# Optimization experiments

Measured on AMD Instinct MI355X. Metric: run time of the kernel, lower is better.

The kernel has to match this reference:

```python
import jax, jax.numpy as jnp
import numpy as np

B, T, D, H, K, V, W = 2, 2048, 768, 12, 64, 64, 1024
EPS = 1e-6


def setup_inputs() -> dict:
    key = jax.random.key(0)
    ks = jax.random.split(key, 10)
    std = 0.02
    return {
        "x": jax.random.normal(ks[0], (B, T, D), jnp.float32),
        "gdn_state": jax.random.normal(ks[1], (B, H, K, V), jnp.float32),
        "Wq": jax.random.normal(ks[2], (D, H * K), jnp.float32) * std,
        "Wk": jax.random.normal(ks[3], (D, H * K), jnp.float32) * std,
        "Wv": jax.random.normal(ks[4], (D, H * K), jnp.float32) * std,
        "Wo": jax.random.normal(ks[5], (H * K, D), jnp.float32) * std,
        "Wgq": jax.random.normal(ks[6], (D, H * K), jnp.float32) * std,
        "Wro": jax.random.normal(ks[7], (H * V, D), jnp.float32) * std,
        "Wg": jax.random.normal(ks[8], (D, H), jnp.float32) * std,
        "bg": jnp.full((H,), 1.0, jnp.float32),  # swa_gate_init
        "norm_w": jnp.ones((D,), jnp.float32),
    }


def reference(x, gdn_state, Wq, Wk, Wv, Wo, Wgq, Wro, Wg, bg, norm_w):
    # RMSNorm
    xn = x * jax.lax.rsqrt(jnp.mean(x * x, axis=-1, keepdims=True) + EPS) * norm_w

    def proj(w):  # (B,T,D)@(D,HK) -> (B,H,T,K)
        return (xn @ w).reshape(B, T, H, K).transpose(0, 2, 1, 3)

    q, k, v = proj(Wq), proj(Wk), proj(Wv)
    scale = K ** -0.5

    scores = jnp.einsum("bhqk,bhsk->bhqs", q, k) * scale  # (B,H,T,T)
    i = jnp.arange(T)[:, None]
    j = jnp.arange(T)[None, :]
    allowed = (j <= i) & (j >= i - W)  # causal sliding window
    scores = jnp.where(allowed, scores, -jnp.inf)
    attn = jax.nn.softmax(scores, axis=-1)

    local = jnp.einsum("bhqs,bhsk->bhqk", attn, v)
    local = local.transpose(0, 2, 1, 3).reshape(B, T, H * K) @ Wo  # (B,T,D)

    # GDN state retrieval
    qg = jax.nn.relu((xn @ Wgq).reshape(B, T, H, K).transpose(0, 2, 1, 3))  # (B,H,T,K)
    retrieved = jnp.einsum("bhkv,bhtk->bhtv", gdn_state, qg)  # (B,H,T,V)
    retrieval = retrieved.transpose(0, 2, 1, 3).reshape(B, T, H * V) @ Wro  # (B,T,D)
    gate = jax.nn.sigmoid(xn @ Wg + bg)  # (B,T,H)
    retrieval = jnp.mean(gate, axis=-1, keepdims=True) * retrieval

    return x + local + retrieval
```

## Files before the change

kernel.cpp:

```cpp
#include <hip/hip_runtime.h>
#include <math.h>
#include <stdint.h>

typedef float f32x4 __attribute__((ext_vector_type(4)));
typedef __bf16 bf16x8 __attribute__((ext_vector_type(8)));
typedef __bf16 bf16x4 __attribute__((ext_vector_type(4)));

constexpr int Bc = 2, Tc = 2048, Dc = 768, Hc = 12, Wc = 1024;
#define CEXP 0.18033688011112042f

__device__ __forceinline__ f32x4 mfma_bf16(bf16x8 a, bf16x8 b, f32x4 c) {
    return __builtin_amdgcn_mfma_f32_16x16x32_bf16(a, b, c, 0, 0, 0);
}
__device__ __forceinline__ void gload16(const void* g, void* l) {
    __builtin_amdgcn_global_load_lds(
        (const __attribute__((address_space(1))) uint32_t*)g,
        (__attribute__((address_space(3))) uint32_t*)l, 16, 0, 0);
}
__device__ __forceinline__ uint32_t pack2(float a, float b) {
    union { __bf16 h[2]; uint32_t u; } x;
    x.h[0] = (__bf16)a; x.h[1] = (__bf16)b; return x.u;
}
__device__ __forceinline__ void s_wait_vm4()   { asm volatile("s_waitcnt vmcnt(4)" ::: "memory"); }
__device__ __forceinline__ void s_wait_vm0()   { asm volatile("s_waitcnt vmcnt(0)" ::: "memory"); }
__device__ __forceinline__ void s_wait_lgkm0() { asm volatile("s_waitcnt lgkmcnt(0)" ::: "memory"); }
__device__ __forceinline__ void bar()          { __builtin_amdgcn_s_barrier(); }

__global__ __launch_bounds__(256) void k_prep_w(
    const float* __restrict__ Wq, const float* __restrict__ Wk,
    const float* __restrict__ Wv, const float* __restrict__ Wgq,
    const float* __restrict__ Wo, const float* __restrict__ Wro,
    __bf16* __restrict__ wTproj, __bf16* __restrict__ wTout)
{
    __shared__ __bf16 ldsT[64][66];
    const int wsel = blockIdx.y;
    const float* srcs[6] = {Wq, Wk, Wv, Wgq, Wo, Wro};
    const float* src = srcs[wsel];
    __bf16* dst; int dstride, koff;
    if (wsel < 4) { dst = wTproj + (size_t)wsel * Dc * Dc; dstride = Dc;  koff = 0; }
    else if (wsel == 4) { dst = wTout; dstride = 1536; koff = 0; }
    else { dst = wTout; dstride = 1536; koff = 768; }
    const float scale = (wsel == 0) ? CEXP : 1.0f;

    int tile = blockIdx.x;
    int tk = tile % 12, tn = tile / 12;
    int k0 = tk * 64, n0 = tn * 64;
    int i = threadIdx.x, rsub = i >> 4, c4 = i & 15;
#pragma unroll
    for (int rep = 0; rep < 4; ++rep) {
        int row = rep * 16 + rsub;
        float4 v = *(const float4*)(src + (size_t)(k0 + row) * Dc + n0 + c4 * 4);
        ldsT[c4 * 4 + 0][row] = (__bf16)(v.x * scale);
        ldsT[c4 * 4 + 1][row] = (__bf16)(v.y * scale);
        ldsT[c4 * 4 + 2][row] = (__bf16)(v.z * scale);
        ldsT[c4 * 4 + 3][row] = (__bf16)(v.w * scale);
    }
    __syncthreads();
#pragma unroll
    for (int rep = 0; rep < 4; ++rep) {
        int n = rep * 16 + rsub;
        bf16x4 o = *(const bf16x4*)&ldsT[n][c4 * 4];
        *(bf16x4*)(dst + (size_t)(n0 + n) * dstride + koff + k0 + c4 * 4) = o;
    }
}

__global__ __launch_bounds__(256) void k_prep_state(
    const float* __restrict__ st, __bf16* __restrict__ stT)
{
    int idx = blockIdx.x * 256 + threadIdx.x;
    int bh = idx >> 12, kk = (idx >> 6) & 63, vv = idx & 63;
    stT[(size_t)bh * 4096 + vv * 64 + kk] = (__bf16)st[idx];
}

__global__ __launch_bounds__(256) void k_rmsnorm(
    const float* __restrict__ x, const float* __restrict__ norm_w,
    __bf16* __restrict__ xnb)
{
    int row = blockIdx.x, tid = threadIdx.x;
    const float* xr = x + (size_t)row * Dc;
    float4 v = make_float4(0.f, 0.f, 0.f, 0.f);
    float ss = 0.f;
    if (tid < 192) {
        v = ((const float4*)xr)[tid];
        ss = v.x * v.x + v.y * v.y + v.z * v.z + v.w * v.w;
    }
#pragma unroll
    for (int m = 32; m; m >>= 1) ss += __shfl_xor(ss, m, 64);
    __shared__ float red[4];
    if ((tid & 63) == 0) red[tid >> 6] = ss;
    __syncthreads();
    float tot = red[0] + red[1] + red[2] + red[3];
    float rms = rsqrtf(tot * (1.f / 768.f) + 1e-6f);
    if (tid < 192) {
        float4 nw = ((const float4*)norm_w)[tid];
        bf16x4 o;
        o[0] = (__bf16)(v.x * rms * nw.x);
        o[1] = (__bf16)(v.y * rms * nw.y);
        o[2] = (__bf16)(v.z * rms * nw.z);
        o[3] = (__bf16)(v.w * rms * nw.w);
        *(bf16x4*)(xnb + (size_t)row * Dc + tid * 4) = o;
    }
}

__global__ __launch_bounds__(256) void k_gate(
    const __bf16* __restrict__ xnb, const float* __restrict__ Wg,
    const float* __restrict__ bg, float* __restrict__ gmean)
{
    int row = blockIdx.x * 4 + (threadIdx.x >> 6);
    int lane = threadIdx.x & 63;
    const __bf16* xr = xnb + (size_t)row * Dc;
    float p[12];
#pragma unroll
    for (int h = 0; h < 12; ++h) p[h] = 0.f;
    for (int d = lane; d < Dc; d += 64) {
        float xv = (float)xr[d];
        const float* wr = Wg + d * 12;
#pragma unroll
        for (int h = 0; h < 12; ++h) p[h] += xv * wr[h];
    }
#pragma unroll
    for (int h = 0; h < 12; ++h) {
#pragma unroll
        for (int m = 32; m; m >>= 1) p[h] += __shfl_xor(p[h], m, 64);
    }
    if (lane == 0) {
        float s = 0.f;
#pragma unroll
        for (int h = 0; h < 12; ++h) s += 1.f / (1.f + expf(-(p[h] + bg[h])));
        gmean[row] = s * (1.f / 12.f);
    }
}

template <int MODE>
__global__ __launch_bounds__(256) void k_gemm(
    const __bf16* __restrict__ A, const __bf16* __restrict__ BT,
    const float* __restrict__ xres, float* __restrict__ outf,
    __bf16* __restrict__ qb, __bf16* __restrict__ kbf,
    __bf16* __restrict__ vtb, __bf16* __restrict__ qgb)
{
    constexpr int BM = (MODE == 0) ? 128 : 64;
    constexpr int BN = (MODE == 0) ? 128 : 64;
    constexpr int KD = (MODE == 0) ? 768 : 1536;
    constexpr int BK = (MODE == 0) ? 32 : 64;
    constexpr int KI = BK / 32;
    constexpr int WM = BM / 2, WN = BN / 2;
    constexpr int MI = WM / 16, NI = WN / 16;
    constexpr int MT = 4096 / BM;
    constexpr int NK = KD / BK;
    constexpr int GR = BK / 8;
    constexpr int ACH = BM * BK / 2048;
    constexpr int BCH = BN * BK / 2048;
    __shared__ __bf16 As[2][BM * BK];
    __shared__ __bf16 Bs[2][BN * BK];
    const int tid = threadIdx.x, w = tid >> 6, lane = tid & 63;
    const int g = lane >> 4, t = lane & 15;
    int id = blockIdx.x, xcd = id & 7, l = id >> 3;
    int nid = xcd * 96 + l;
    int m0 = (nid % MT) * BM, n0 = (nid / MT) * BN;
    const __bf16* Abase = A + (size_t)m0 * KD;
    const __bf16* Bbase = BT + (size_t)n0 * KD;
    const int wrow = (w >> 1) * WM, wcol = (w & 1) * WN;

    auto STAGE = [&](int buf, int k0) {
#pragma unroll
        for (int c = 0; c < ACH; ++c) {
            int chunk = c * 256 + tid, row = chunk / GR, cix = chunk % GR;
            gload16(Abase + (size_t)row * KD + k0 + cix * 8, &As[buf][chunk * 8]);
        }
#pragma unroll
        for (int c = 0; c < BCH; ++c) {
            int chunk = c * 256 + tid, row = chunk / GR, cix = chunk % GR;
            gload16(Bbase + (size_t)row * KD + k0 + cix * 8, &Bs[buf][chunk * 8]);
        }
    };

    f32x4 acc[MI][NI] = {};
    STAGE(0, 0);
    STAGE(1, BK);
    for (int ks = 0; ks < NK; ++ks) {
        if (ks == NK - 1) s_wait_vm0(); else s_wait_vm4();
        bar();
        const __bf16* Ab = As[ks & 1];
        const __bf16* Bb = Bs[ks & 1];
        bf16x8 af[MI][KI], bfr[NI][KI];
#pragma unroll
        for (int kk = 0; kk < KI; ++kk) {
#pragma unroll
            for (int mi = 0; mi < MI; ++mi)
                af[mi][kk] = *(const bf16x8*)(Ab + (wrow + mi * 16 + t) * BK + kk * 32 + g * 8);
#pragma unroll
            for (int ni = 0; ni < NI; ++ni)
                bfr[ni][kk] = *(const bf16x8*)(Bb + (wcol + ni * 16 + t) * BK + kk * 32 + g * 8);
        }
        s_wait_lgkm0();
        __builtin_amdgcn_sched_barrier(0);
        bar();
        if (ks + 2 < NK) STAGE(ks & 1, (ks + 2) * BK);
        __builtin_amdgcn_s_setprio(1);
#pragma unroll
        for (int kk = 0; kk < KI; ++kk)
#pragma unroll
            for (int mi = 0; mi < MI; ++mi)
#pragma unroll
                for (int ni = 0; ni < NI; ++ni)
                    acc[mi][ni] = mfma_bf16(af[mi][kk], bfr[ni][kk], acc[mi][ni]);
        __builtin_amdgcn_s_setprio(0);
    }
    const int region = (MODE == 0) ? (n0 / 768) : 0;
#pragma unroll
    for (int mi = 0; mi < MI; ++mi)
#pragma unroll
        for (int ni = 0; ni < NI; ++ni)
#pragma unroll
            for (int r = 0; r < 4; ++r) {
                int grow = m0 + wrow + mi * 16 + g * 4 + r;
                int gcol = n0 + wcol + ni * 16 + t;
                float v = acc[mi][ni][r];
                if (MODE == 1) {
                    size_t idx = (size_t)grow * Dc + gcol;
                    outf[idx] = xres[idx] + v;
                } else {
                    int c = gcol - region * 768;
                    int h = c >> 6, kd = c & 63;
                    int b = grow >> 11, ti = grow & (Tc - 1);
                    if (region == 0)
                        qb[((size_t)(b * Hc + h) * Tc + ti) * 64 + kd] = (__bf16)v;
                    else if (region == 1) {
                        int kds = kd ^ ((ti & 7) << 3);
                        kbf[((size_t)(b * Hc + h) * Tc + ti) * 64 + kds] = (__bf16)v;
                    } else if (region == 2) {
                        int kap = ti & 63;
                        int rho = (kap & 32) | (((kap >> 2) & 3) << 3) |
                                  (((kap >> 4) & 1) << 2) | (kap & 3);
                        int ts = (ti & ~63) | (rho ^ ((kd & 7) << 3));
                        vtb[((size_t)(b * Hc + h) * 64 + kd) * Tc + ts] = (__bf16)v;
                    } else
                        qgb[((size_t)(b * Hc + h) * Tc + ti) * 64 + kd] = (__bf16)fmaxf(v, 0.f);
                }
            }
}

__global__ __launch_bounds__(256) void k_attn(
    const __bf16* __restrict__ q, const __bf16* __restrict__ k,
    const __bf16* __restrict__ vt, __bf16* __restrict__ ac)
{
    __shared__ __bf16 Ks[2][64 * 64];
    __shared__ __bf16 Vs[2][64 * 64];
    int id = blockIdx.x, xcd = id & 7, l = id >> 3;
    int nid = xcd * 96 + l;
    int sblk = nid & 31, h = (nid >> 5) % Hc, b = nid / (32 * Hc);
    int tid = threadIdx.x;
    int w = tid >> 6, lane = tid & 63;
    int g = lane >> 4, t = lane & 15;
    int q0 = sblk * 64, qw = q0 + w * 16;
    const __bf16* qb = q + (size_t)(b * Hc + h) * Tc * 64;
    const __bf16* kb = k + (size_t)(b * Hc + h) * Tc * 64;
    const __bf16* vb = vt + (size_t)(b * Hc + h) * 64 * Tc;

    bf16x8 qf0 = *(const bf16x8*)(qb + (size_t)(qw + t) * 64 + g * 8);
    bf16x8 qf1 = *(const bf16x8*)(qb + (size_t)(qw + t) * 64 + 32 + g * 8);

    const int qi = qw + t;
    const int lowB = qi - Wc;
    const int xr = t & 7;

    f32x4 oacc[4] = {};
    float lsum = 0.f;

    const int s_begin = (q0 >= Wc) ? q0 - Wc : 0;
    const int s_endq = q0 + 64;

    auto STAGE = [&](int buf, int s0) {
#pragma unroll
        for (int j = 0; j < 2; ++j) {
            int ch = j * 256 + tid;
            gload16(kb + (size_t)(s0 + (ch >> 3)) * 64 + (ch & 7) * 8,
                    &Ks[buf][ch * 8]);
            gload16(vb + (size_t)(ch >> 3) * Tc + s0 + (ch & 7) * 8,
                    &Vs[buf][ch * 8]);
        }
    };

    STAGE(0, s_begin);
    if (s_begin + 64 < s_endq) STAGE(1, s_begin + 64);
    int cur = 0;
    for (int s0 = s_begin; s0 < s_endq; s0 += 64) {
        if (s0 + 64 >= s_endq) s_wait_vm0(); else s_wait_vm4();
        bar();
        const __bf16* Kt = Ks[cur];
        const __bf16* Vt = Vs[cur];
        f32x4 sc[4];
        __builtin_amdgcn_s_setprio(1);
#pragma unroll
        for (int sub = 0; sub < 4; ++sub) {
            const __bf16* kr = Kt + (sub * 16 + t) * 64;
            bf16x8 kA = *(const bf16x8*)(kr + ((g ^ xr) << 3));
            bf16x8 kB = *(const bf16x8*)(kr + (((g + 4) ^ xr) << 3));
            f32x4 s = {};
            s = mfma_bf16(kA, qf0, s);
            s = mfma_bf16(kB, qf1, s);
            sc[sub] = s;
        }
        __builtin_amdgcn_s_setprio(0);
        float pv[4][4];
#pragma unroll
        for (int sub = 0; sub < 4; ++sub)
#pragma unroll
            for (int r = 0; r < 4; ++r) {
                int kk = s0 + sub * 16 + g * 4 + r;
                float e = exp2f(sc[sub][r]);
                float val = (kk <= qi && kk >= lowB) ? e : 0.f;
                pv[sub][r] = val;
                lsum += val;
            }
        __builtin_amdgcn_s_setprio(1);
#pragma unroll
        for (int ks = 0; ks < 2; ++ks) {
            union { uint32_t u[4]; bf16x8 v; } pf;
            pf.u[0] = pack2(pv[ks * 2][0], pv[ks * 2][1]);
            pf.u[1] = pack2(pv[ks * 2][2], pv[ks * 2][3]);
            pf.u[2] = pack2(pv[ks * 2 + 1][0], pv[ks * 2 + 1][1]);
            pf.u[3] = pack2(pv[ks * 2 + 1][2], pv[ks * 2 + 1][3]);
#pragma unroll
            for (int n = 0; n < 4; ++n) {
                const __bf16* vrow = Vt + (n * 16 + t) * 64;
                bf16x8 vf = *(const bf16x8*)(vrow + ((((ks * 4) + g) ^ xr) << 3));
                oacc[n] = mfma_bf16(pf.v, vf, oacc[n]);
            }
        }
        __builtin_amdgcn_s_setprio(0);
        s_wait_lgkm0();
        __builtin_amdgcn_sched_barrier(0);
        bar();
        if (s0 + 128 < s_endq) STAGE(cur, s0 + 128);
        cur ^= 1;
    }
    lsum += __shfl_xor(lsum, 16, 64);
    lsum += __shfl_xor(lsum, 32, 64);
    float linv = 1.f / lsum;
    float lq[4];
#pragma unroll
    for (int r = 0; r < 4; ++r) lq[r] = __shfl(linv, g * 4 + r, 64);
#pragma unroll
    for (int n = 0; n < 4; ++n)
#pragma unroll
        for (int r = 0; r < 4; ++r) {
            int qrow = qw + g * 4 + r;
            ac[(size_t)(b * Tc + qrow) * 1536 + h * 64 + n * 16 + t] =
                (__bf16)(oacc[n][r] * lq[r]);
        }
}

__global__ __launch_bounds__(256) void k_retr(
    const __bf16* __restrict__ qg, const __bf16* __restrict__ stateT,
    const float* __restrict__ gmean, __bf16* __restrict__ ac)
{
    int b = blockIdx.z, h = blockIdx.y;
    int w = threadIdx.x >> 6, lane = threadIdx.x & 63;
    int g = lane >> 4, t = lane & 15;
    int t0 = blockIdx.x * 64 + w * 16;
    const __bf16* qbp = qg + (size_t)(b * Hc + h) * Tc * 64;
    const __bf16* sb = stateT + (size_t)(b * Hc + h) * 64 * 64;
    bf16x8 a0 = *(const bf16x8*)(qbp + (size_t)(t0 + t) * 64 + g * 8);
    bf16x8 a1 = *(const bf16x8*)(qbp + (size_t)(t0 + t) * 64 + 32 + g * 8);
#pragma unroll
    for (int n = 0; n < 4; ++n) {
        bf16x8 b0 = *(const bf16x8*)(sb + (n * 16 + t) * 64 + g * 8);
        bf16x8 b1 = *(const bf16x8*)(sb + (n * 16 + t) * 64 + 32 + g * 8);
        f32x4 acc = {};
        acc = mfma_bf16(a0, b0, acc);
        acc = mfma_bf16(a1, b1, acc);
#pragma unroll
        for (int r = 0; r < 4; ++r) {
            int ti = t0 + g * 4 + r;
            float gm = gmean[b * Tc + ti];
            ac[(size_t)(b * Tc + ti) * 1536 + 768 + h * 64 + n * 16 + t] =
                (__bf16)(acc[r] * gm);
        }
    }
}

extern "C" void kernel_launch(void* const* d_in, const int* in_sizes, int n_in,
                              void* d_out, int out_size, void* d_ws, size_t ws_size,
                              hipStream_t stream) {
    (void)in_sizes; (void)n_in; (void)out_size; (void)ws_size;
    const float* x     = (const float*)d_in[0];
    const float* gdn   = (const float*)d_in[1];
    const float* Wq    = (const float*)d_in[2];
    const float* Wk    = (const float*)d_in[3];
    const float* Wv    = (const float*)d_in[4];
    const float* Wo    = (const float*)d_in[5];
    const float* Wgq   = (const float*)d_in[6];
    const float* Wro   = (const float*)d_in[7];
    const float* Wg    = (const float*)d_in[8];
    const float* bg    = (const float*)d_in[9];
    const float* normw = (const float*)d_in[10];
    float* out = (float*)d_out;

    char* p = (char*)d_ws;
    auto alloc = [&](size_t bytes) -> char* {
        char* r = p; p += (bytes + 255) & ~(size_t)255; return r;
    };
    constexpr size_t NROW = (size_t)Bc * Tc;
    __bf16* xnb    = (__bf16*)alloc(NROW * Dc * 2);
    __bf16* wTproj = (__bf16*)alloc((size_t)4 * Dc * Dc * 2);
    __bf16* wTout  = (__bf16*)alloc((size_t)Dc * 1536 * 2);
    __bf16* stT    = (__bf16*)alloc((size_t)Bc * Hc * 64 * 64 * 2);
    __bf16* qbuf   = (__bf16*)alloc(NROW * Dc * 2);
    __bf16* kbuf   = (__bf16*)alloc(NROW * Dc * 2);
    __bf16* qgbuf  = (__bf16*)alloc(NROW * Dc * 2);
    __bf16* vtbuf  = (__bf16*)alloc(NROW * Dc * 2);
    __bf16* ac     = (__bf16*)alloc(NROW * 1536 * 2);
    float*  gmean  = (float*)alloc(NROW * 4);

    k_prep_w<<<dim3(144, 6), 256, 0, stream>>>(Wq, Wk, Wv, Wgq, Wo, Wro, wTproj, wTout);
    k_prep_state<<<(Bc * Hc * 64 * 64) / 256, 256, 0, stream>>>(gdn, stT);
    k_rmsnorm<<<NROW, 256, 0, stream>>>(x, normw, xnb);
    k_gate<<<NROW / 4, 256, 0, stream>>>(xnb, Wg, bg, gmean);

    k_gemm<0><<<768, 256, 0, stream>>>(xnb, wTproj, nullptr, nullptr,
                                       qbuf, kbuf, vtbuf, qgbuf);
    k_attn<<<768, 256, 0, stream>>>(qbuf, kbuf, vtbuf, ac);
    k_retr<<<dim3(Tc / 64, Hc, Bc), 256, 0, stream>>>(qgbuf, stT, gmean, ac);
    k_gemm<1><<<768, 256, 0, stream>>>(ac, wTout, x, out,
                                       nullptr, nullptr, nullptr, nullptr);
}
```

Before: 131.0 us.

## Triple-buffer GEMM and attention tile loads; transpose gate weights for coalescing

The GEMM and sliding-window attention kernels move from double to triple buffering in LDS, keeping two tiles of global-to-LDS loads in flight, with vmcnt waits chosen from the number of outstanding tiles. This is meant to hide more global-load latency behind the MFMA work. A small new kernel transposes the gate weight Wg so the gate kernel's loads are contiguous across lanes instead of strided by 12. The extra LDS per block may lower occupancy, and the added launch carries its own overhead.

```diff
diff --git a/kernel.cpp b/kernel.cpp
--- a/kernel.cpp
+++ b/kernel.cpp
@@ -21,10 +21,16 @@
     union { __bf16 h[2]; uint32_t u; } x;
     x.h[0] = (__bf16)a; x.h[1] = (__bf16)b; return x.u;
 }
+__device__ __forceinline__ void s_wait_vm8()   { asm volatile("s_waitcnt vmcnt(8)" ::: "memory"); }
 __device__ __forceinline__ void s_wait_vm4()   { asm volatile("s_waitcnt vmcnt(4)" ::: "memory"); }
 __device__ __forceinline__ void s_wait_vm0()   { asm volatile("s_waitcnt vmcnt(0)" ::: "memory"); }
 __device__ __forceinline__ void s_wait_lgkm0() { asm volatile("s_waitcnt lgkmcnt(0)" ::: "memory"); }
 __device__ __forceinline__ void bar()          { __builtin_amdgcn_s_barrier(); }
+__device__ __forceinline__ void wait_tiles(int infl) {
+    if (infl >= 2) s_wait_vm8();
+    else if (infl == 1) s_wait_vm4();
+    else s_wait_vm0();
+}
 
 __global__ __launch_bounds__(256) void k_prep_w(
     const float* __restrict__ Wq, const float* __restrict__ Wk,
@@ -70,6 +76,14 @@
     int idx = blockIdx.x * 256 + threadIdx.x;
     int bh = idx >> 12, kk = (idx >> 6) & 63, vv = idx & 63;
     stT[(size_t)bh * 4096 + vv * 64 + kk] = (__bf16)st[idx];
+}
+
+__global__ __launch_bounds__(256) void k_prep_wgt(
+    const float* __restrict__ Wg, float* __restrict__ WgT)
+{
+    int i = blockIdx.x * 256 + threadIdx.x;
+    int h = i / Dc, d = i - h * Dc;
+    WgT[i] = Wg[d * 12 + h];
 }
 
 __global__ __launch_bounds__(256) void k_rmsnorm(
@@ -103,7 +117,7 @@
 }
 
 __global__ __launch_bounds__(256) void k_gate(
-    const __bf16* __restrict__ xnb, const float* __restrict__ Wg,
+    const __bf16* __restrict__ xnb, const float* __restrict__ WgT,
     const float* __restrict__ bg, float* __restrict__ gmean)
 {
     int row = blockIdx.x * 4 + (threadIdx.x >> 6);
@@ -114,9 +128,8 @@
     for (int h = 0; h < 12; ++h) p[h] = 0.f;
     for (int d = lane; d < Dc; d += 64) {
         float xv = (float)xr[d];
-        const float* wr = Wg + d * 12;
-#pragma unroll
-        for (int h = 0; h < 12; ++h) p[h] += xv * wr[h];
+#pragma unroll
+        for (int h = 0; h < 12; ++h) p[h] += xv * WgT[h * Dc + d];
     }
 #pragma unroll
     for (int h = 0; h < 12; ++h) {
@@ -150,8 +163,8 @@
     constexpr int GR = BK / 8;
     constexpr int ACH = BM * BK / 2048;
     constexpr int BCH = BN * BK / 2048;
-    __shared__ __bf16 As[2][BM * BK];
-    __shared__ __bf16 Bs[2][BN * BK];
+    __shared__ __bf16 As[3][BM * BK];
+    __shared__ __bf16 Bs[3][BN * BK];
     const int tid = threadIdx.x, w = tid >> 6, lane = tid & 63;
     const int g = lane >> 4, t = lane & 15;
     int id = blockIdx.x, xcd = id & 7, l = id >> 3;
@@ -177,11 +190,13 @@
     f32x4 acc[MI][NI] = {};
     STAGE(0, 0);
     STAGE(1, BK);
+    STAGE(2, 2 * BK);
+    int buf = 0;
     for (int ks = 0; ks < NK; ++ks) {
-        if (ks == NK - 1) s_wait_vm0(); else s_wait_vm4();
+        wait_tiles(NK - 1 - ks);
         bar();
-        const __bf16* Ab = As[ks & 1];
-        const __bf16* Bb = Bs[ks & 1];
+        const __bf16* Ab = As[buf];
+        const __bf16* Bb = Bs[buf];
         bf16x8 af[MI][KI], bfr[NI][KI];
 #pragma unroll
         for (int kk = 0; kk < KI; ++kk) {
@@ -195,7 +210,8 @@
         s_wait_lgkm0();
         __builtin_amdgcn_sched_barrier(0);
         bar();
-        if (ks + 2 < NK) STAGE(ks & 1, (ks + 2) * BK);
+        if (ks + 3 < NK) STAGE(buf, (ks + 3) * BK);
+        buf = (buf == 2) ? 0 : buf + 1;
         __builtin_amdgcn_s_setprio(1);
 #pragma unroll
         for (int kk = 0; kk < KI; ++kk)
@@ -244,8 +260,8 @@
     const __bf16* __restrict__ q, const __bf16* __restrict__ k,
     const __bf16* __restrict__ vt, __bf16* __restrict__ ac)
 {
-    __shared__ __bf16 Ks[2][64 * 64];
-    __shared__ __bf16 Vs[2][64 * 64];
+    __shared__ __bf16 Ks[3][64 * 64];
+    __shared__ __bf16 Vs[3][64 * 64];
     int id = blockIdx.x, xcd = id & 7, l = id >> 3;
     int nid = xcd * 96 + l;
     int sblk = nid & 31, h = (nid >> 5) % Hc, b = nid / (32 * Hc);
@@ -268,7 +284,7 @@
     float lsum = 0.f;
 
     const int s_begin = (q0 >= Wc) ? q0 - Wc : 0;
-    const int s_endq = q0 + 64;
+    const int NT = (q0 + 64 - s_begin) >> 6;
 
     auto STAGE = [&](int buf, int s0) {
 #pragma unroll
@@ -282,13 +298,15 @@
     };
 
     STAGE(0, s_begin);
-    if (s_begin + 64 < s_endq) STAGE(1, s_begin + 64);
-    int cur = 0;
-    for (int s0 = s_begin; s0 < s_endq; s0 += 64) {
-        if (s0 + 64 >= s_endq) s_wait_vm0(); else s_wait_vm4();
+    if (NT > 1) STAGE(1, s_begin + 64);
+    if (NT > 2) STAGE(2, s_begin + 128);
+    int buf = 0;
+    for (int it = 0; it < NT; ++it) {
+        int s0 = s_begin + it * 64;
+        wait_tiles(NT - 1 - it);
         bar();
-        const __bf16* Kt = Ks[cur];
-        const __bf16* Vt = Vs[cur];
+        const __bf16* Kt = Ks[buf];
+        const __bf16* Vt = Vs[buf];
         f32x4 sc[4];
         __builtin_amdgcn_s_setprio(1);
 #pragma unroll
@@ -332,8 +350,8 @@
         s_wait_lgkm0();
         __builtin_amdgcn_sched_barrier(0);
         bar();
-        if (s0 + 128 < s_endq) STAGE(cur, s0 + 128);
-        cur ^= 1;
+        if (it + 3 < NT) STAGE(buf, s0 + 192);
+        buf = (buf == 2) ? 0 : buf + 1;
     }
     lsum += __shfl_xor(lsum, 16, 64);
     lsum += __shfl_xor(lsum, 32, 64);
@@ -412,11 +430,13 @@
     __bf16* vtbuf  = (__bf16*)alloc(NROW * Dc * 2);
     __bf16* ac     = (__bf16*)alloc(NROW * 1536 * 2);
     float*  gmean  = (float*)alloc(NROW * 4);
+    float*  WgT    = (float*)alloc((size_t)12 * Dc * 4);
 
     k_prep_w<<<dim3(144, 6), 256, 0, stream>>>(Wq, Wk, Wv, Wgq, Wo, Wro, wTproj, wTout);
     k_prep_state<<<(Bc * Hc * 64 * 64) / 256, 256, 0, stream>>>(gdn, stT);
+    k_prep_wgt<<<36, 256, 0, stream>>>(Wg, WgT);
     k_rmsnorm<<<NROW, 256, 0, stream>>>(x, normw, xnb);
-    k_gate<<<NROW / 4, 256, 0, stream>>>(xnb, Wg, bg, gmean);
+    k_gate<<<NROW / 4, 256, 0, stream>>>(xnb, WgT, bg, gmean);
 
     k_gemm<0><<<768, 256, 0, stream>>>(xnb, wTproj, nullptr, nullptr,
                                        qbuf, kbuf, vtbuf, qgbuf);
```

Result: slower. 138.0 us (+5.3%).
